# Kernel optimization log

Measured on AMD Instinct MI355X. Metric: run time of the kernel, lower is better.

Reference implementation:

```python
import jax, jax.numpy as jnp
import numpy as np

EPS = 0.001   # EPSILON2
T1 = 1.0
T2 = 100.0
DISC = 16     # number of discrete features
B, F, K1, K2 = 524288, 16, 16, 8


def _enforce(v):
    # Enforced autograd fn: forward = max(v, EPS), backward = identity (STE)
    return v + jax.lax.stop_gradient(jnp.maximum(v, EPS) - v)


def _soft_bin(cont, interval, i_min):
    """cont: [B,F]; interval: [F,K]; i_min: [F]. Vectorized over features/bins.
    Returns (STE one-hot out [B, F*K], kmeans_loss scalar)."""
    # bin centers = i_min + running cumsum of (enforced) gaps -> [F,K]
    centers = i_min[:, None] + jnp.cumsum(_enforce(interval), axis=1)
    d = (cont[:, :, None] - centers[None, :, :]) ** 2          # [B,F,K]
    s1 = jax.nn.softmax(-T1 * d, axis=-1)                      # kmeans softmax
    kmeans_loss = jnp.sum(jnp.mean(jnp.sum(d * s1, axis=-1), axis=0))
    s2 = jax.nn.softmax(-T2 * d, axis=-1)                      # sharp softmax
    oh = jax.nn.one_hot(jnp.argmax(s2, axis=-1), d.shape[-1], dtype=s2.dtype)
    out = s2 + jax.lax.stop_gradient(oh - s2)                  # STE one-hot
    return out.reshape(cont.shape[0], -1), kmeans_loss


def setup_inputs() -> dict:
    key = jax.random.key(0)
    k1, k2, k3 = jax.random.split(key, 3)
    x = jax.random.uniform(k1, (B, DISC + F), dtype=jnp.float32)
    interval = jax.random.uniform(k2, (F, K1), dtype=jnp.float32,
                                  minval=0.01, maxval=0.12)
    interval2 = jax.random.uniform(k3, (F, K2), dtype=jnp.float32,
                                   minval=0.02, maxval=0.2)
    i_min = jnp.zeros((F,), dtype=jnp.float32)
    return {"x": x, "interval": interval, "interval2": interval2, "i_min": i_min}


def reference(x, interval, interval2, i_min):
    x_disc, cont = x[:, :DISC], x[:, DISC:]
    out1, loss1 = _soft_bin(cont, interval, i_min)
    out2, loss2 = _soft_bin(cont, interval2, i_min)
    total_out = jnp.concatenate([x_disc, out1, out2], axis=1)  # [B, DISC+F*(K1+K2)]
    return total_out, loss1 + loss2
```

## Files before the change

kernel.cpp:

```cpp
#include <hip/hip_runtime.h>


constexpr int kB      = 524288;
constexpr int kF      = 16;
constexpr int kK1     = 16;
constexpr int kK2     = 8;
constexpr int kRowIn  = 32;
constexpr int kRowOut = 400;
constexpr float kEps  = 0.001f;
constexpr int kTPB    = 256;
constexpr int kC4     = kRowOut / 4;
constexpr int kXStride = 33;

template <int K>
__device__ __forceinline__ int soft_argmax_loss(const float* __restrict__ dd,
                                                double& lacc)
{
#pragma clang fp contract(off)
    float se = 0.f, sde = 0.f;
#pragma unroll
    for (int k = 0; k < K; ++k) {
        float e = expf(-dd[k]);
        se += e; sde += dd[k] * e;
    }
    lacc += (double)(sde / se);

    float z[K];
#pragma unroll
    for (int k = 0; k < K; ++k) z[k] = -100.0f * dd[k];
    float m = z[0];
#pragma unroll
    for (int k = 1; k < K; ++k) m = fmaxf(m, z[k]);
    float e2[K]; float ss = 0.f;
#pragma unroll
    for (int k = 0; k < K; ++k) { e2[k] = expf(z[k] - m); ss += e2[k]; }

    int kmax = 0; float emax = e2[0];
#pragma unroll
    for (int k = 1; k < K; ++k) {
        if (e2[k] > emax) { emax = e2[k]; kmax = k; }
    }

    bool cand = false;
#pragma unroll
    for (int k = 0; k < K; ++k)
        cand |= (k < kmax) & (e2[k] >= emax * 0.99999964f);
    if (cand) {
        float pmax = emax / ss;
        for (int j = 0; j < kmax; ++j) {
            if (e2[j] / ss == pmax) { kmax = j; break; }
        }
    }
    return kmax;
}

__global__ __launch_bounds__(kTPB) void binlayer_main(
    const float* __restrict__ x,
    const float* __restrict__ interval,
    const float* __restrict__ interval2,
    const float* __restrict__ i_min,
    float* __restrict__ out,
    double* __restrict__ loss_acc)
{
#pragma clang fp contract(off)
    __shared__ float sC1[kF][kK1];
    __shared__ float sC2[kF][kK2];
    __shared__ float sX[kTPB * kXStride];
    __shared__ unsigned char sIdx[kTPB * kF];

    const int tid = threadIdx.x;

    if (tid < kF) {
        const float base = i_min[tid];
        float run = 0.f;
        for (int k = 0; k < kK1; ++k) {
            run += fmaxf(interval[tid * kK1 + k], kEps);
            sC1[tid][k] = base + run;
        }
        run = 0.f;
        for (int k = 0; k < kK2; ++k) {
            run += fmaxf(interval2[tid * kK2 + k], kEps);
            sC2[tid][k] = base + run;
        }
    }

    const long long rowBase = (long long)blockIdx.x * kTPB;

    const float4* __restrict__ xin4 = (const float4*)(x + rowBase * kRowIn);
#pragma unroll
    for (int i = 0; i < (kTPB * kRowIn / 4) / kTPB; ++i) {
        int flat = i * kTPB + tid;
        float4 v = xin4[flat];
        int r = flat >> 3, c4 = flat & 7;
        float* p = &sX[r * kXStride + c4 * 4];
        p[0] = v.x; p[1] = v.y; p[2] = v.z; p[3] = v.w;
    }
    __syncthreads();

    double lacc = 0.0;
    const float* __restrict__ myc = &sX[tid * kXStride + 16];

#pragma unroll 1
    for (int f = 0; f < kF; ++f) {
        const float c = myc[f];

        float dd1[kK1];
#pragma unroll
        for (int k = 0; k < kK1; ++k) { float t = c - sC1[f][k]; dd1[k] = t * t; }
        int k1 = soft_argmax_loss<kK1>(dd1, lacc);

        float dd2[kK2];
#pragma unroll
        for (int k = 0; k < kK2; ++k) { float t = c - sC2[f][k]; dd2[k] = t * t; }
        int k2 = soft_argmax_loss<kK2>(dd2, lacc);

        sIdx[tid * kF + f] = (unsigned char)(k1 | (k2 << 4));
    }

#pragma unroll
    for (int off = 32; off > 0; off >>= 1) lacc += __shfl_down(lacc, off);
    if ((tid & 63) == 0) atomicAdd(loss_acc, lacc);

    __syncthreads();

    float4* __restrict__ o4 = (float4*)(out + rowBase * kRowOut);
#pragma unroll 1
    for (int i = 0; i < kC4; ++i) {
        unsigned idx = (unsigned)(i * kTPB + tid);
        unsigned r = idx / 100u;
        unsigned c = idx - r * 100u;
        float4 o;
        if (c < 4u) {
            const float* p = &sX[r * kXStride + c * 4u];
            o.x = p[0]; o.y = p[1]; o.z = p[2]; o.w = p[3];
        } else if (c < 68u) {
            unsigned u = c - 4u, f = u >> 2, q = (u & 3u) * 4u;
            unsigned k = sIdx[r * kF + f] & 15u;
            o.x = (k == q + 0u) ? 1.f : 0.f;
            o.y = (k == q + 1u) ? 1.f : 0.f;
            o.z = (k == q + 2u) ? 1.f : 0.f;
            o.w = (k == q + 3u) ? 1.f : 0.f;
        } else {
            unsigned u = c - 68u, f = u >> 1, q = (u & 1u) * 4u;
            unsigned k = (unsigned)(sIdx[r * kF + f]) >> 4;
            o.x = (k == q + 0u) ? 1.f : 0.f;
            o.y = (k == q + 1u) ? 1.f : 0.f;
            o.z = (k == q + 2u) ? 1.f : 0.f;
            o.w = (k == q + 3u) ? 1.f : 0.f;
        }
        o4[idx] = o;
    }
}

__global__ void binlayer_finalize(const double* __restrict__ acc,
                                  float* __restrict__ out)
{
    out[(long long)kB * kRowOut] = (float)(*acc * (1.0 / (double)kB));
}

extern "C" void kernel_launch(void* const* d_in, const int* in_sizes, int n_in,
                              void* d_out, int out_size, void* d_ws, size_t ws_size,
                              hipStream_t stream)
{
    const float* x    = (const float*)d_in[0];
    const float* itv1 = (const float*)d_in[1];
    const float* itv2 = (const float*)d_in[2];
    const float* imin = (const float*)d_in[3];
    float* out = (float*)d_out;
    double* acc = (double*)d_ws;

    hipMemsetAsync(acc, 0, sizeof(double), stream);
    binlayer_main<<<kB / kTPB, kTPB, 0, stream>>>(x, itv1, itv2, imin, out, acc);
    binlayer_finalize<<<1, 1, 0, stream>>>(acc, out);
}
```

Before: 961.3 us.

## Skip sharp-softmax exps via logit argmax, fast exp, per-block loss partials

Finds the argmax directly on the scaled logits, so the sharp softmax exponentials only run in the rare near-tie case, and switches the k-means exp to the fast __expf intrinsic. It also replaces the per-wavefront double atomicAdd and the memset with per-block partial sums written to workspace, reduced by a 256-thread finalize kernel. This trims ALU work and atomic contention, but the kernel is dominated by writing the large output, so the gain may be limited. The fast exp and the changed tie handling could slightly perturb the loss or tie-breaking.

```diff
diff --git a/kernel.cpp b/kernel.cpp
--- a/kernel.cpp
+++ b/kernel.cpp
@@ -9,6 +9,7 @@
 constexpr int kRowOut = 400;
 constexpr float kEps  = 0.001f;
 constexpr int kTPB    = 256;
+constexpr int kGrid   = kB / kTPB;
 constexpr int kC4     = kRowOut / 4;
 constexpr int kXStride = 33;
 
@@ -20,7 +21,7 @@
     float se = 0.f, sde = 0.f;
 #pragma unroll
     for (int k = 0; k < K; ++k) {
-        float e = expf(-dd[k]);
+        float e = __expf(-dd[k]);
         se += e; sde += dd[k] * e;
     }
     lacc += (double)(sde / se);
@@ -28,28 +29,25 @@
     float z[K];
 #pragma unroll
     for (int k = 0; k < K; ++k) z[k] = -100.0f * dd[k];
-    float m = z[0];
-#pragma unroll
-    for (int k = 1; k < K; ++k) m = fmaxf(m, z[k]);
-    float e2[K]; float ss = 0.f;
-#pragma unroll
-    for (int k = 0; k < K; ++k) { e2[k] = expf(z[k] - m); ss += e2[k]; }
-
-    int kmax = 0; float emax = e2[0];
+    float m = z[0]; int kmax = 0;
 #pragma unroll
     for (int k = 1; k < K; ++k) {
-        if (e2[k] > emax) { emax = e2[k]; kmax = k; }
+        if (z[k] > m) { m = z[k]; kmax = k; }
     }
 
     bool cand = false;
 #pragma unroll
     for (int k = 0; k < K; ++k)
-        cand |= (k < kmax) & (e2[k] >= emax * 0.99999964f);
+        cand |= (k < kmax) & (z[k] >= m - 2.4e-7f);
     if (cand) {
-        float pmax = emax / ss;
-        for (int j = 0; j < kmax; ++j) {
-            if (e2[j] / ss == pmax) { kmax = j; break; }
+        float e2[K]; float ss = 0.f;
+        for (int k = 0; k < K; ++k) { e2[k] = expf(z[k] - m); ss += e2[k]; }
+        int km = 0; float pmax = e2[0] / ss;
+        for (int k = 1; k < K; ++k) {
+            float p = e2[k] / ss;
+            if (p > pmax) { pmax = p; km = k; }
         }
+        kmax = km;
     }
     return kmax;
 }
@@ -60,13 +58,14 @@
     const float* __restrict__ interval2,
     const float* __restrict__ i_min,
     float* __restrict__ out,
-    double* __restrict__ loss_acc)
+    double* __restrict__ partial)
 {
 #pragma clang fp contract(off)
     __shared__ float sC1[kF][kK1];
     __shared__ float sC2[kF][kK2];
     __shared__ float sX[kTPB * kXStride];
     __shared__ unsigned char sIdx[kTPB * kF];
+    __shared__ double sL[kTPB / 64];
 
     const int tid = threadIdx.x;
 
@@ -119,9 +118,11 @@
 
 #pragma unroll
     for (int off = 32; off > 0; off >>= 1) lacc += __shfl_down(lacc, off);
-    if ((tid & 63) == 0) atomicAdd(loss_acc, lacc);
+    if ((tid & 63) == 0) sL[tid >> 6] = lacc;
 
     __syncthreads();
+
+    if (tid == 0) partial[blockIdx.x] = sL[0] + sL[1] + sL[2] + sL[3];
 
     float4* __restrict__ o4 = (float4*)(out + rowBase * kRowOut);
 #pragma unroll 1
@@ -152,10 +153,23 @@
     }
 }
 
-__global__ void binlayer_finalize(const double* __restrict__ acc,
-                                  float* __restrict__ out)
+__global__ __launch_bounds__(256) void binlayer_finalize(
+    const double* __restrict__ partial,
+    float* __restrict__ out)
 {
-    out[(long long)kB * kRowOut] = (float)(*acc * (1.0 / (double)kB));
+    __shared__ double sL[4];
+    const int tid = threadIdx.x;
+    double s = 0.0;
+#pragma unroll
+    for (int i = 0; i < kGrid / 256; ++i)
+        s += partial[i * 256 + tid];
+#pragma unroll
+    for (int off = 32; off > 0; off >>= 1) s += __shfl_down(s, off);
+    if ((tid & 63) == 0) sL[tid >> 6] = s;
+    __syncthreads();
+    if (tid == 0)
+        out[(long long)kB * kRowOut] =
+            (float)((sL[0] + sL[1] + sL[2] + sL[3]) * (1.0 / (double)kB));
 }
 
 extern "C" void kernel_launch(void* const* d_in, const int* in_sizes, int n_in,
@@ -167,9 +181,8 @@
     const float* itv2 = (const float*)d_in[2];
     const float* imin = (const float*)d_in[3];
     float* out = (float*)d_out;
-    double* acc = (double*)d_ws;
+    double* partial = (double*)d_ws;
 
-    hipMemsetAsync(acc, 0, sizeof(double), stream);
-    binlayer_main<<<kB / kTPB, kTPB, 0, stream>>>(x, itv1, itv2, imin, out, acc);
-    binlayer_finalize<<<1, 1, 0, stream>>>(acc, out);
+    binlayer_main<<<kGrid, kTPB, 0, stream>>>(x, itv1, itv2, imin, out, partial);
+    binlayer_finalize<<<1, 256, 0, stream>>>(partial, out);
 }
```

After: 891.5 us. 7.3% less time.
